# Kernel optimization log

Measured on AMD Instinct MI355X. Metric: run time of the kernel, lower is better.

The kernel has to match this reference:

```python
import jax, jax.numpy as jnp
import numpy as np

B, S, D_IN, D_OUT, H = 4, 2048, 768, 768, 12
DH = D_OUT // H


def setup_inputs() -> dict:
    key = jax.random.key(0)
    ks = jax.random.split(key, 6)
    x = jax.random.normal(ks[0], (B, S, D_IN), dtype=jnp.float32)
    # causal mask: True above the diagonal means "masked out" (filled with -inf)
    mask = jnp.triu(jnp.ones((S, S), dtype=bool), k=1)
    sc = 1.0 / np.sqrt(D_IN)
    Wq = jax.random.normal(ks[1], (D_IN, D_OUT), dtype=jnp.float32) * sc
    Wk = jax.random.normal(ks[2], (D_IN, D_OUT), dtype=jnp.float32) * sc
    Wv = jax.random.normal(ks[3], (D_IN, D_OUT), dtype=jnp.float32) * sc
    Wo = jax.random.normal(ks[4], (D_OUT, D_OUT), dtype=jnp.float32) * (1.0 / np.sqrt(D_OUT))
    bo = jnp.zeros((D_OUT,), dtype=jnp.float32)
    return {"input_tensor": x, "mask": mask, "Wq": Wq, "Wk": Wk, "Wv": Wv, "Wo": Wo, "bo": bo}


def reference(input_tensor, mask, Wq, Wk, Wv, Wo, bo):
    b, n, _ = input_tensor.shape
    # projections -> [b, h, n, dh]
    q = (input_tensor @ Wq).reshape(b, n, H, DH).transpose(0, 2, 1, 3)
    k = (input_tensor @ Wk).reshape(b, n, H, DH).transpose(0, 2, 1, 3)
    v = (input_tensor @ Wv).reshape(b, n, H, DH).transpose(0, 2, 1, 3)
    # scores [b, h, n, n]
    scores = jnp.einsum('bhqd,bhkd->bhqk', q, k)
    scores = jnp.where(mask[:n, :n], -jnp.inf, scores)
    attn = jax.nn.softmax(scores / np.sqrt(DH), axis=-1)
    ctx = jnp.einsum('bhqk,bhkd->bhqd', attn, v)
    ctx = ctx.transpose(0, 2, 1, 3).reshape(b, n, D_OUT)
    return ctx @ Wo + bo
```

## Files before the change

### kernel.cpp

```cpp
#include <hip/hip_runtime.h>
#include <hip/hip_bf16.h>
#include <math.h>

typedef __attribute__((ext_vector_type(4))) float f32x4;
typedef __attribute__((ext_vector_type(8))) short s16x8;
typedef __attribute__((ext_vector_type(8))) unsigned short u16x8;

#define B_ 4
#define S_ 2048
#define DIN 768
#define DOUT 768
#define H_ 12
#define DH_ 64
#define M_ (B_*S_)

__device__ __forceinline__ unsigned short f2bf(float f) {
  union { float f; unsigned u; } v; v.f = f;
  unsigned r = v.u + 0x7fffu + ((v.u >> 16) & 1u);
  return (unsigned short)(r >> 16);
}

#if __has_builtin(__builtin_amdgcn_exp2f)
#define EXP2(x) __builtin_amdgcn_exp2f(x)
#else
#define EXP2(x) exp2f(x)
#endif


__global__ __launch_bounds__(256) void prep(
    const float* __restrict__ X, unsigned short* __restrict__ Xb,
    const float* __restrict__ W0, const float* __restrict__ W1,
    const float* __restrict__ W2, const float* __restrict__ W3,
    unsigned short* __restrict__ Wt)
{
  __shared__ float t[32][33];
  const int bid = blockIdx.x;
  if (bid < 3072) {
    size_t i = ((size_t)bid * 256 + threadIdx.x) * 8;
    float4 a = *(const float4*)&X[i];
    float4 b = *(const float4*)&X[i + 4];
    u16x8 v;
    v[0] = f2bf(a.x); v[1] = f2bf(a.y); v[2] = f2bf(a.z); v[3] = f2bf(a.w);
    v[4] = f2bf(b.x); v[5] = f2bf(b.y); v[6] = f2bf(b.z); v[7] = f2bf(b.w);
    *(u16x8*)&Xb[i] = v;
  } else {
    const int t4 = bid - 3072;
    const int z = t4 / 576, rem = t4 - z * 576;
    const int ky = rem / 24, nx = rem - ky * 24;
    const float* W = z == 0 ? W0 : z == 1 ? W1 : z == 2 ? W2 : W3;
    unsigned short* Out = Wt + (size_t)z * DOUT * DIN;
    const int n0 = nx * 32, k0 = ky * 32;
    const int tx = threadIdx.x & 31, ty = threadIdx.x >> 5;
#pragma unroll
    for (int i = 0; i < 32; i += 8)
      t[ty + i][tx] = W[(size_t)(k0 + ty + i) * DOUT + n0 + tx];
    __syncthreads();
#pragma unroll
    for (int i = 0; i < 32; i += 8)
      Out[(size_t)(n0 + ty + i) * DIN + k0 + tx] = f2bf(t[tx][ty + i]);
  }
}


#define BKC 64
#define TILE_E (128 * BKC)

__device__ __forceinline__ void stage_tile(
    const unsigned short* __restrict__ g, int row0, int k0,
    unsigned short* lds, int tid)
{
#pragma unroll
  for (int it = 0; it < 4; ++it) {
    int s = it * 256 + tid;
    int row = s >> 3, sc = s & 7;
    int gc = sc ^ (row & 7);
    const unsigned short* gsrc = g + (size_t)(row0 + row) * 768 + k0 + gc * 8;
    unsigned short* dst = lds + (size_t)(it * 256 + (tid & ~63)) * 8;
    __builtin_amdgcn_global_load_lds(
        (const __attribute__((address_space(1))) void*)gsrc,
        (__attribute__((address_space(3))) void*)dst, 16, 0, 0);
  }
}

__device__ __forceinline__ void gemm_core(
    const unsigned short* __restrict__ A, const unsigned short* __restrict__ Bt,
    int m0, int n0, unsigned short* As, unsigned short* Bs,
    f32x4 acc[4][4], int tid)
{
  const int lane = tid & 63;
  const int col_l = lane & 15, quad = lane >> 4;
  const int w = tid >> 6;
  const int wm = (w & 1) * 64, wn = (w >> 1) * 64;

  stage_tile(A, m0, 0, As, tid);
  stage_tile(Bt, n0, 0, Bs, tid);

#pragma unroll 2
  for (int k0 = 0; k0 < 768; k0 += BKC) {
    const int cur = (k0 >> 6) & 1;
    const unsigned short* Asb = As + cur * TILE_E;
    const unsigned short* Bsb = Bs + cur * TILE_E;
    if (k0 + BKC < 768) {
      stage_tile(A, m0, k0 + BKC, As + (cur ^ 1) * TILE_E, tid);
      stage_tile(Bt, n0, k0 + BKC, Bs + (cur ^ 1) * TILE_E, tid);
      asm volatile("s_waitcnt vmcnt(8)" ::: "memory");
    } else {
      asm volatile("s_waitcnt vmcnt(0)" ::: "memory");
    }
    __builtin_amdgcn_s_barrier();

#pragma unroll
    for (int kk = 0; kk < 2; ++kk) {
      s16x8 af[4], bf[4];
#pragma unroll
      for (int t = 0; t < 4; ++t) {
        int ar = wm + t * 16 + col_l;
        af[t] = *(const s16x8*)&Asb[ar * BKC + (((kk << 2) + quad) ^ (ar & 7)) * 8];
        int br = wn + t * 16 + col_l;
        bf[t] = *(const s16x8*)&Bsb[br * BKC + (((kk << 2) + quad) ^ (br & 7)) * 8];
      }
#pragma unroll
      for (int mt = 0; mt < 4; ++mt)
#pragma unroll
        for (int nt = 0; nt < 4; ++nt)
          acc[mt][nt] = __builtin_amdgcn_mfma_f32_16x16x32_bf16(
              af[mt], bf[nt], acc[mt][nt], 0, 0, 0);
    }

    __builtin_amdgcn_s_barrier();
  }
}

__global__ __launch_bounds__(256) void proj_mfma(
    const unsigned short* __restrict__ Xb, const unsigned short* __restrict__ Wt,
    unsigned short* __restrict__ Qo, unsigned short* __restrict__ Ko,
    unsigned short* __restrict__ Vo)
{
  __shared__ unsigned short As[2 * TILE_E];
  __shared__ unsigned short Bs[2 * TILE_E];
  const int tid = threadIdx.x;

  const int orig = (blockIdx.z * 64 + blockIdx.y) * 6 + blockIdx.x;
  const int id = (orig & 7) * 144 + (orig >> 3);
  const int z = id / 384;
  const int r = id - z * 384;
  const int my = r / 6, nx = r - my * 6;
  const int m0 = my * 128, n0 = nx * 128;

  const unsigned short* Bw = Wt + (size_t)z * DOUT * DIN;
  unsigned short* Out = z == 0 ? Qo : z == 1 ? Ko : Vo;
  const float scale = z == 0 ? 0.125f * 1.44269504f : 1.0f;

  f32x4 acc[4][4] = {};
  gemm_core(Xb, Bw, m0, n0, As, Bs, acc, tid);

  const int lane = tid & 63, w = tid >> 6;
  const int col_l = lane & 15, quad = lane >> 4;
  const int wm = (w & 1) * 64, wn = (w >> 1) * 64;
  if (z == 2) {
    const int mblk = m0 + wm;
    const int b = mblk >> 11, sblk = mblk & (S_ - 1);
#pragma unroll
    for (int mt = 0; mt < 4; ++mt) {
      const int slot = (mt >> 1) * 32 + quad * 8 + (mt & 1) * 4;
#pragma unroll
      for (int nt = 0; nt < 4; ++nt) {
        int n = n0 + wn + nt * 16 + col_l;
        int h = n >> 6, d = n & 63;
        ushort4 v;
        v.x = f2bf(acc[mt][nt][0]); v.y = f2bf(acc[mt][nt][1]);
        v.z = f2bf(acc[mt][nt][2]); v.w = f2bf(acc[mt][nt][3]);
        *(ushort4*)&Out[((size_t)(b * H_ + h) * DH_ + d) * S_ + sblk + slot] = v;
      }
    }
  } else {
#pragma unroll
    for (int mt = 0; mt < 4; ++mt)
#pragma unroll
      for (int nt = 0; nt < 4; ++nt) {
        int n = n0 + wn + nt * 16 + col_l;
        int h = n >> 6, d = n & 63;
#pragma unroll
        for (int r2 = 0; r2 < 4; ++r2) {
          int m = m0 + wm + mt * 16 + quad * 4 + r2;
          int b = m >> 11, s = m & (S_ - 1);
          Out[((size_t)(b * H_ + h) * S_ + s) * DH_ + d] = f2bf(acc[mt][nt][r2] * scale);
        }
      }
  }
}

__global__ __launch_bounds__(256) void out_mfma(
    const unsigned short* __restrict__ Cb, const unsigned short* __restrict__ Wt,
    const float* __restrict__ bo, float* __restrict__ Out)
{
  __shared__ unsigned short As[2 * TILE_E];
  __shared__ unsigned short Bs[2 * TILE_E];
  const int tid = threadIdx.x;

  const int orig = blockIdx.y * 6 + blockIdx.x;
  const int id = (orig & 7) * 48 + (orig >> 3);
  const int my = id / 6, nx = id - my * 6;
  const int m0 = my * 128, n0 = nx * 128;

  f32x4 acc[4][4] = {};
  gemm_core(Cb, Wt, m0, n0, As, Bs, acc, tid);

  const int lane = tid & 63, w = tid >> 6;
  const int col_l = lane & 15, quad = lane >> 4;
  const int wm = (w & 1) * 64, wn = (w >> 1) * 64;
#pragma unroll
  for (int mt = 0; mt < 4; ++mt)
#pragma unroll
    for (int nt = 0; nt < 4; ++nt) {
      int n = n0 + wn + nt * 16 + col_l;
      float bias = bo[n];
#pragma unroll
      for (int r = 0; r < 4; ++r) {
        int m = m0 + wm + mt * 16 + quad * 4 + r;
        Out[(size_t)m * DOUT + n] = acc[mt][nt][r] + bias;
      }
    }
}


union PK { uint2 u2[2]; s16x8 v; };

#define MFMA_BF16 __builtin_amdgcn_mfma_f32_16x16x32_bf16

__device__ __forceinline__ void exppack(const f32x4 sc[4], PK& p0, PK& p1) {
#pragma unroll
  for (int nc = 0; nc < 4; ++nc) {
    float e0 = EXP2(sc[nc][0] - 17.3123405f);
    float e1 = EXP2(sc[nc][1] - 17.3123405f);
    float e2 = EXP2(sc[nc][2] - 17.3123405f);
    float e3 = EXP2(sc[nc][3] - 17.3123405f);
    union { __hip_bfloat162 v; unsigned u; } lo, hi;
    lo.v = __float22bfloat162_rn(make_float2(e0, e1));
    hi.v = __float22bfloat162_rn(make_float2(e2, e3));
    uint2 pw; pw.x = lo.u; pw.y = hi.u;
    if (nc < 2) p0.u2[nc] = pw; else p1.u2[nc - 2] = pw;
  }
}

__device__ __forceinline__ void stage_kv(
    const unsigned short* __restrict__ Kg, const unsigned short* __restrict__ Vg,
    int jn, unsigned short* KsB, unsigned short* VsB, int tid)
{
#pragma unroll
  for (int it = 0; it < 2; ++it) {
    int s = it * 256 + tid;
    int row = s >> 3;
    int gc = ((s & 7) ^ (row & 7)) * 8;
    unsigned short* dst = KsB + (size_t)(it * 256 + (tid & ~63)) * 8;
    __builtin_amdgcn_global_load_lds(
        (const __attribute__((address_space(1))) void*)(Kg + (size_t)(jn + row) * DH_ + gc),
        (__attribute__((address_space(3))) void*)dst, 16, 0, 0);
  }
#pragma unroll
  for (int it = 0; it < 2; ++it) {
    int s = it * 256 + tid;
    int row = s >> 3;
    int gc = ((s & 7) ^ (row & 7)) * 8;
    unsigned short* dst = VsB + (size_t)(it * 256 + (tid & ~63)) * 8;
    __builtin_amdgcn_global_load_lds(
        (const __attribute__((address_space(1))) void*)(Vg + (size_t)row * S_ + jn + gc),
        (__attribute__((address_space(3))) void*)dst, 16, 0, 0);
  }
}

__global__ __launch_bounds__(256, 3) void attn_mfma(
    const unsigned short* __restrict__ Q, const unsigned short* __restrict__ K,
    const unsigned short* __restrict__ Vt, unsigned short* __restrict__ CTX)
{
  __shared__ unsigned short Ks[2][64 * 64];
  __shared__ unsigned short Vs[2][64 * 64];

  const int tid = threadIdx.x;
  const int lane = tid & 63;
  const int w = tid >> 6;
  const int col_l = lane & 15;
  const int quad = lane >> 4;

  const int orig = (blockIdx.z * 12 + blockIdx.y) * 16 + blockIdx.x;
  const int id = (orig & 7) * 96 + (orig >> 3);
  const int p = id & 15;
  const int bh = id >> 4;
  const int h = bh % 12, b = bh / 12;

  const int q0A = p << 6, q0B = (31 - p) << 6;
  const int ntiles = 32 - p;
  const size_t bhs = (size_t)(b * H_ + h);
  const unsigned short* Qg = Q + bhs * S_ * DH_;
  const unsigned short* Kg = K + bhs * S_ * DH_;
  const unsigned short* Vg = Vt + bhs * DH_ * S_;

  const int qwA = q0A + (w << 4), qwB = q0B + (w << 4);
  s16x8 aqA0 = *(const s16x8*)&Qg[(size_t)(qwA + col_l) * DH_ + quad * 8];
  s16x8 aqA1 = *(const s16x8*)&Qg[(size_t)(qwA + col_l) * DH_ + 32 + quad * 8];
  s16x8 aqB0 = *(const s16x8*)&Qg[(size_t)(qwB + col_l) * DH_ + quad * 8];
  s16x8 aqB1 = *(const s16x8*)&Qg[(size_t)(qwB + col_l) * DH_ + 32 + quad * 8];

  stage_kv(Kg, Vg, 0, &Ks[0][0], &Vs[0][0], tid);

  f32x4 oA[4] = {}, oB[4] = {}, lA = {}, lB = {};
  s16x8 bones;
#pragma unroll
  for (int i = 0; i < 8; ++i) bones[i] = (short)0x3F80;

  const int qrel = (w << 4) + col_l;
  const int r7 = col_l & 7;

  for (int t = 0; t < ntiles; ++t) {
    if (t + 1 < ntiles) {
      stage_kv(Kg, Vg, (t + 1) << 6, &Ks[(t + 1) & 1][0], &Vs[(t + 1) & 1][0], tid);
      asm volatile("s_waitcnt vmcnt(4)" ::: "memory");
    } else {
      asm volatile("s_waitcnt vmcnt(0)" ::: "memory");
    }
    __builtin_amdgcn_s_barrier();

    const unsigned short* KsB = &Ks[t & 1][0];
    const unsigned short* VsB = &Vs[t & 1][0];
    const bool doA = (t <= p);

    f32x4 scA[4], scB[4];
    __builtin_amdgcn_s_setprio(1);
#pragma unroll
    for (int nc = 0; nc < 4; ++nc) {
      const int kr = nc * 16 + col_l;
      s16x8 k0 = *(const s16x8*)&KsB[kr * 64 + ((quad ^ r7) * 8)];
      s16x8 k1 = *(const s16x8*)&KsB[kr * 64 + (((quad + 4) ^ r7) * 8)];
      f32x4 a = {};
      a = MFMA_BF16(k0, aqB0, a, 0, 0, 0);
      a = MFMA_BF16(k1, aqB1, a, 0, 0, 0);
      scB[nc] = a;
      if (doA) {
        f32x4 c = {};
        c = MFMA_BF16(k0, aqA0, c, 0, 0, 0);
        c = MFMA_BF16(k1, aqA1, c, 0, 0, 0);
        scA[nc] = c;
      }
    }
    __builtin_amdgcn_s_setprio(0);
    if (t == p) {
#pragma unroll
      for (int nc = 0; nc < 4; ++nc)
#pragma unroll
        for (int r = 0; r < 4; ++r)
          if (nc * 16 + quad * 4 + r > qrel) scA[nc][r] = -INFINITY;
    }
    if (t == ntiles - 1) {
#pragma unroll
      for (int nc = 0; nc < 4; ++nc)
#pragma unroll
        for (int r = 0; r < 4; ++r)
          if (nc * 16 + quad * 4 + r > qrel) scB[nc][r] = -INFINITY;
    }

    PK pA0, pA1, pB0, pB1;
    if (doA) exppack(scA, pA0, pA1);
    exppack(scB, pB0, pB1);

    __builtin_amdgcn_s_setprio(1);
#pragma unroll
    for (int dc = 0; dc < 4; ++dc) {
      const int vr = dc * 16 + col_l;
      s16x8 b0 = *(const s16x8*)&VsB[vr * 64 + ((quad ^ r7) * 8)];
      s16x8 b1 = *(const s16x8*)&VsB[vr * 64 + (((quad + 4) ^ r7) * 8)];
      oB[dc] = MFMA_BF16(pB0.v, b0, oB[dc], 0, 0, 0);
      oB[dc] = MFMA_BF16(pB1.v, b1, oB[dc], 0, 0, 0);
      if (doA) {
        oA[dc] = MFMA_BF16(pA0.v, b0, oA[dc], 0, 0, 0);
        oA[dc] = MFMA_BF16(pA1.v, b1, oA[dc], 0, 0, 0);
      }
    }
    lB = MFMA_BF16(pB0.v, bones, lB, 0, 0, 0);
    lB = MFMA_BF16(pB1.v, bones, lB, 0, 0, 0);
    if (doA) {
      lA = MFMA_BF16(pA0.v, bones, lA, 0, 0, 0);
      lA = MFMA_BF16(pA1.v, bones, lA, 0, 0, 0);
    }
    __builtin_amdgcn_s_setprio(0);

    __builtin_amdgcn_s_barrier();
  }

  float liA[4], liB[4];
#pragma unroll
  for (int r = 0; r < 4; ++r) {
    liA[r] = 1.0f / lA[r];
    liB[r] = 1.0f / lB[r];
  }
#pragma unroll
  for (int dc = 0; dc < 4; ++dc)
#pragma unroll
    for (int r = 0; r < 4; ++r) {
      CTX[((size_t)(b * S_ + qwA + quad * 4 + r)) * DOUT + h * DH_ + dc * 16 + col_l]
          = f2bf(oA[dc][r] * liA[r]);
      CTX[((size_t)(b * S_ + qwB + quad * 4 + r)) * DOUT + h * DH_ + dc * 16 + col_l]
          = f2bf(oB[dc][r] * liB[r]);
    }
}


extern "C" void kernel_launch(void* const* d_in, const int* in_sizes, int n_in,
                              void* d_out, int out_size, void* d_ws, size_t ws_size,
                              hipStream_t stream) {
  const float* X  = (const float*)d_in[0];
  const float* Wq = (const float*)d_in[2];
  const float* Wk = (const float*)d_in[3];
  const float* Wv = (const float*)d_in[4];
  const float* Wo = (const float*)d_in[5];
  const float* bo = (const float*)d_in[6];
  float* out = (float*)d_out;

  unsigned short* Xb = (unsigned short*)d_ws;
  unsigned short* Wt = Xb + (size_t)M_ * DIN;
  unsigned short* Qb = Wt + (size_t)4 * DOUT * DIN;
  unsigned short* Kb = Qb + (size_t)M_ * DOUT;
  unsigned short* Vb = Kb + (size_t)M_ * DOUT;
  unsigned short* Cb = Vb + (size_t)M_ * DOUT;

  prep<<<dim3(3072 + 2304), 256, 0, stream>>>(X, Xb, Wq, Wk, Wv, Wo, Wt);
  proj_mfma<<<dim3(DOUT / 128, M_ / 128, 3), 256, 0, stream>>>(Xb, Wt, Qb, Kb, Vb);
  attn_mfma<<<dim3(16, H_, B_), 256, 0, stream>>>(Qb, Kb, Vb, Cb);
  out_mfma<<<dim3(DOUT / 128, M_ / 128), 256, 0, stream>>>(
      Cb, Wt + (size_t)3 * DOUT * DIN, bo, out);
}
```

Before: 196.6 us.

## Software-pipeline attention loop with triple-buffered K/V and lookahead QK+exp

Restructures the attention main loop so the QK^T scores and exponentials for tile t+1 are computed in the same iteration as the PV accumulation for tile t. K/V shared-memory staging becomes triple-buffered with a prefetch distance of two tiles, and the trailing barrier is dropped in favour of one wait+barrier per iteration. The aim is to overlap the exp/VALU work with the MFMA work and to hide global-to-LDS load latency. The cost is more LDS (three buffers instead of two) and more live registers for two sets of packed probabilities, which may reduce occupancy under the 3-blocks-per-SM launch bound. A full vmcnt(0) wait each iteration may also serialise loads.

```diff
diff --git a/kernel.cpp b/kernel.cpp
--- a/kernel.cpp
+++ b/kernel.cpp
@@ -269,12 +269,55 @@
   }
 }
 
+__device__ __forceinline__ void qk_exp(
+    const unsigned short* KsB,
+    s16x8 aqA0, s16x8 aqA1, s16x8 aqB0, s16x8 aqB1,
+    bool dA, bool maskA, bool maskB, int qrel, int col_l, int quad, int r7,
+    PK& pA0, PK& pA1, PK& pB0, PK& pB1)
+{
+  f32x4 scA[4], scB[4];
+  __builtin_amdgcn_s_setprio(1);
+#pragma unroll
+  for (int nc = 0; nc < 4; ++nc) {
+    const int kr = nc * 16 + col_l;
+    s16x8 k0 = *(const s16x8*)&KsB[kr * 64 + ((quad ^ r7) * 8)];
+    s16x8 k1 = *(const s16x8*)&KsB[kr * 64 + (((quad + 4) ^ r7) * 8)];
+    f32x4 a = {};
+    a = MFMA_BF16(k0, aqB0, a, 0, 0, 0);
+    a = MFMA_BF16(k1, aqB1, a, 0, 0, 0);
+    scB[nc] = a;
+    if (dA) {
+      f32x4 c = {};
+      c = MFMA_BF16(k0, aqA0, c, 0, 0, 0);
+      c = MFMA_BF16(k1, aqA1, c, 0, 0, 0);
+      scA[nc] = c;
+    }
+  }
+  __builtin_amdgcn_s_setprio(0);
+  if (maskA) {
+#pragma unroll
+    for (int nc = 0; nc < 4; ++nc)
+#pragma unroll
+      for (int r = 0; r < 4; ++r)
+        if (nc * 16 + quad * 4 + r > qrel) scA[nc][r] = -INFINITY;
+  }
+  if (maskB) {
+#pragma unroll
+    for (int nc = 0; nc < 4; ++nc)
+#pragma unroll
+      for (int r = 0; r < 4; ++r)
+        if (nc * 16 + quad * 4 + r > qrel) scB[nc][r] = -INFINITY;
+  }
+  if (dA) exppack(scA, pA0, pA1);
+  exppack(scB, pB0, pB1);
+}
+
 __global__ __launch_bounds__(256, 3) void attn_mfma(
     const unsigned short* __restrict__ Q, const unsigned short* __restrict__ K,
     const unsigned short* __restrict__ Vt, unsigned short* __restrict__ CTX)
 {
-  __shared__ unsigned short Ks[2][64 * 64];
-  __shared__ unsigned short Vs[2][64 * 64];
+  __shared__ unsigned short Ks[3][64 * 64];
+  __shared__ unsigned short Vs[3][64 * 64];
 
   const int tid = threadIdx.x;
   const int lane = tid & 63;
@@ -301,89 +344,66 @@
   s16x8 aqB0 = *(const s16x8*)&Qg[(size_t)(qwB + col_l) * DH_ + quad * 8];
   s16x8 aqB1 = *(const s16x8*)&Qg[(size_t)(qwB + col_l) * DH_ + 32 + quad * 8];
 
+  const int qrel = (w << 4) + col_l;
+  const int r7 = col_l & 7;
+
   stage_kv(Kg, Vg, 0, &Ks[0][0], &Vs[0][0], tid);
+  stage_kv(Kg, Vg, 64, &Ks[1][0], &Vs[1][0], tid);
+  asm volatile("s_waitcnt vmcnt(4)" ::: "memory");
+  __builtin_amdgcn_s_barrier();
+
+  PK cA0, cA1, cB0, cB1;
+  PK nA0, nA1, nB0, nB1;
+  qk_exp(&Ks[0][0], aqA0, aqA1, aqB0, aqB1,
+         true, (p == 0), (ntiles == 1),
+         qrel, col_l, quad, r7, cA0, cA1, cB0, cB1);
 
   f32x4 oA[4] = {}, oB[4] = {}, lA = {}, lB = {};
   s16x8 bones;
 #pragma unroll
   for (int i = 0; i < 8; ++i) bones[i] = (short)0x3F80;
 
-  const int qrel = (w << 4) + col_l;
-  const int r7 = col_l & 7;
+  int bc = 0, bn = 1, bs = 2;
 
   for (int t = 0; t < ntiles; ++t) {
-    if (t + 1 < ntiles) {
-      stage_kv(Kg, Vg, (t + 1) << 6, &Ks[(t + 1) & 1][0], &Vs[(t + 1) & 1][0], tid);
-      asm volatile("s_waitcnt vmcnt(4)" ::: "memory");
-    } else {
-      asm volatile("s_waitcnt vmcnt(0)" ::: "memory");
-    }
+    asm volatile("s_waitcnt vmcnt(0)" ::: "memory");
     __builtin_amdgcn_s_barrier();
 
-    const unsigned short* KsB = &Ks[t & 1][0];
-    const unsigned short* VsB = &Vs[t & 1][0];
-    const bool doA = (t <= p);
-
-    f32x4 scA[4], scB[4];
-    __builtin_amdgcn_s_setprio(1);
-#pragma unroll
-    for (int nc = 0; nc < 4; ++nc) {
-      const int kr = nc * 16 + col_l;
-      s16x8 k0 = *(const s16x8*)&KsB[kr * 64 + ((quad ^ r7) * 8)];
-      s16x8 k1 = *(const s16x8*)&KsB[kr * 64 + (((quad + 4) ^ r7) * 8)];
-      f32x4 a = {};
-      a = MFMA_BF16(k0, aqB0, a, 0, 0, 0);
-      a = MFMA_BF16(k1, aqB1, a, 0, 0, 0);
-      scB[nc] = a;
-      if (doA) {
-        f32x4 c = {};
-        c = MFMA_BF16(k0, aqA0, c, 0, 0, 0);
-        c = MFMA_BF16(k1, aqA1, c, 0, 0, 0);
-        scA[nc] = c;
-      }
-    }
-    __builtin_amdgcn_s_setprio(0);
-    if (t == p) {
-#pragma unroll
-      for (int nc = 0; nc < 4; ++nc)
-#pragma unroll
-        for (int r = 0; r < 4; ++r)
-          if (nc * 16 + quad * 4 + r > qrel) scA[nc][r] = -INFINITY;
-    }
-    if (t == ntiles - 1) {
-#pragma unroll
-      for (int nc = 0; nc < 4; ++nc)
-#pragma unroll
-        for (int r = 0; r < 4; ++r)
-          if (nc * 16 + quad * 4 + r > qrel) scB[nc][r] = -INFINITY;
-    }
-
-    PK pA0, pA1, pB0, pB1;
-    if (doA) exppack(scA, pA0, pA1);
-    exppack(scB, pB0, pB1);
-
+    if (t + 2 < ntiles)
+      stage_kv(Kg, Vg, (t + 2) << 6, &Ks[bs][0], &Vs[bs][0], tid);
+
+    const bool dA_c = (t <= p);
+
+    if (t + 1 < ntiles)
+      qk_exp(&Ks[bn][0], aqA0, aqA1, aqB0, aqB1,
+             (t + 1 <= p), (t + 1 == p),
+             (t + 1 == ntiles - 1),
+             qrel, col_l, quad, r7, nA0, nA1, nB0, nB1);
+
+    const unsigned short* VsB = &Vs[bc][0];
     __builtin_amdgcn_s_setprio(1);
 #pragma unroll
     for (int dc = 0; dc < 4; ++dc) {
       const int vr = dc * 16 + col_l;
       s16x8 b0 = *(const s16x8*)&VsB[vr * 64 + ((quad ^ r7) * 8)];
       s16x8 b1 = *(const s16x8*)&VsB[vr * 64 + (((quad + 4) ^ r7) * 8)];
-      oB[dc] = MFMA_BF16(pB0.v, b0, oB[dc], 0, 0, 0);
-      oB[dc] = MFMA_BF16(pB1.v, b1, oB[dc], 0, 0, 0);
-      if (doA) {
-        oA[dc] = MFMA_BF16(pA0.v, b0, oA[dc], 0, 0, 0);
-        oA[dc] = MFMA_BF16(pA1.v, b1, oA[dc], 0, 0, 0);
+      oB[dc] = MFMA_BF16(cB0.v, b0, oB[dc], 0, 0, 0);
+      oB[dc] = MFMA_BF16(cB1.v, b1, oB[dc], 0, 0, 0);
+      if (dA_c) {
+        oA[dc] = MFMA_BF16(cA0.v, b0, oA[dc], 0, 0, 0);
+        oA[dc] = MFMA_BF16(cA1.v, b1, oA[dc], 0, 0, 0);
       }
     }
-    lB = MFMA_BF16(pB0.v, bones, lB, 0, 0, 0);
-    lB = MFMA_BF16(pB1.v, bones, lB, 0, 0, 0);
-    if (doA) {
-      lA = MFMA_BF16(pA0.v, bones, lA, 0, 0, 0);
-      lA = MFMA_BF16(pA1.v, bones, lA, 0, 0, 0);
+    lB = MFMA_BF16(cB0.v, bones, lB, 0, 0, 0);
+    lB = MFMA_BF16(cB1.v, bones, lB, 0, 0, 0);
+    if (dA_c) {
+      lA = MFMA_BF16(cA0.v, bones, lA, 0, 0, 0);
+      lA = MFMA_BF16(cA1.v, bones, lA, 0, 0, 0);
     }
     __builtin_amdgcn_s_setprio(0);
 
-    __builtin_amdgcn_s_barrier();
+    cA0 = nA0; cA1 = nA1; cB0 = nB0; cB1 = nB1;
+    int tmp = bc; bc = bn; bn = bs; bs = tmp;
   }
 
   float liA[4], liB[4];
```

Result: no change. 199.7 us (+1.5%).

## Serialize paired query tiles into uniform 33-iteration loop instead of sharing K/V tiles

Applied to the files above, without the earlier changes.

Each block handles two causal query tiles (p and 31-p). Before, the kernel streamed 32-p K/V tiles once and computed both tiles against the shared ones. Now it runs a fixed 33 iterations: first all tiles for the B query block, then p+1 tiles again for the A query block. This gives every block an identical trip count and a single MFMA chain per iteration, which cuts divergence and register pressure. The cost is reloading p+1 K/V tiles from global memory, where before they were reused for both query tiles.

```diff
diff --git a/kernel.cpp b/kernel.cpp
--- a/kernel.cpp
+++ b/kernel.cpp
@@ -289,7 +289,8 @@
   const int h = bh % 12, b = bh / 12;
 
   const int q0A = p << 6, q0B = (31 - p) << 6;
-  const int ntiles = 32 - p;
+  const int nB = 32 - p;
+  const int NIT = 33;
   const size_t bhs = (size_t)(b * H_ + h);
   const unsigned short* Qg = Q + bhs * S_ * DH_;
   const unsigned short* Kg = K + bhs * S_ * DH_;
@@ -311,75 +312,83 @@
   const int qrel = (w << 4) + col_l;
   const int r7 = col_l & 7;
 
-  for (int t = 0; t < ntiles; ++t) {
-    if (t + 1 < ntiles) {
-      stage_kv(Kg, Vg, (t + 1) << 6, &Ks[(t + 1) & 1][0], &Vs[(t + 1) & 1][0], tid);
+  for (int i = 0; i < NIT; ++i) {
+    const int buf = i & 1;
+    if (i + 1 < NIT) {
+      const int jn_next = (i + 1 < nB ? i + 1 : i + 1 - nB) << 6;
+      stage_kv(Kg, Vg, jn_next, &Ks[buf ^ 1][0], &Vs[buf ^ 1][0], tid);
       asm volatile("s_waitcnt vmcnt(4)" ::: "memory");
     } else {
       asm volatile("s_waitcnt vmcnt(0)" ::: "memory");
     }
     __builtin_amdgcn_s_barrier();
 
-    const unsigned short* KsB = &Ks[t & 1][0];
-    const unsigned short* VsB = &Vs[t & 1][0];
-    const bool doA = (t <= p);
-
-    f32x4 scA[4], scB[4];
+    const unsigned short* KsB = &Ks[buf][0];
+    const unsigned short* VsB = &Vs[buf][0];
+    const bool isB = i < nB;
+
+    f32x4 sc[4];
     __builtin_amdgcn_s_setprio(1);
-#pragma unroll
-    for (int nc = 0; nc < 4; ++nc) {
-      const int kr = nc * 16 + col_l;
-      s16x8 k0 = *(const s16x8*)&KsB[kr * 64 + ((quad ^ r7) * 8)];
-      s16x8 k1 = *(const s16x8*)&KsB[kr * 64 + (((quad + 4) ^ r7) * 8)];
-      f32x4 a = {};
-      a = MFMA_BF16(k0, aqB0, a, 0, 0, 0);
-      a = MFMA_BF16(k1, aqB1, a, 0, 0, 0);
-      scB[nc] = a;
-      if (doA) {
-        f32x4 c = {};
-        c = MFMA_BF16(k0, aqA0, c, 0, 0, 0);
-        c = MFMA_BF16(k1, aqA1, c, 0, 0, 0);
-        scA[nc] = c;
+    if (isB) {
+#pragma unroll
+      for (int nc = 0; nc < 4; ++nc) {
+        const int kr = nc * 16 + col_l;
+        s16x8 k0 = *(const s16x8*)&KsB[kr * 64 + ((quad ^ r7) * 8)];
+        s16x8 k1 = *(const s16x8*)&KsB[kr * 64 + (((quad + 4) ^ r7) * 8)];
+        f32x4 a = {};
+        a = MFMA_BF16(k0, aqB0, a, 0, 0, 0);
+        a = MFMA_BF16(k1, aqB1, a, 0, 0, 0);
+        sc[nc] = a;
+      }
+    } else {
+#pragma unroll
+      for (int nc = 0; nc < 4; ++nc) {
+        const int kr = nc * 16 + col_l;
+        s16x8 k0 = *(const s16x8*)&KsB[kr * 64 + ((quad ^ r7) * 8)];
+        s16x8 k1 = *(const s16x8*)&KsB[kr * 64 + (((quad + 4) ^ r7) * 8)];
+        f32x4 a = {};
+        a = MFMA_BF16(k0, aqA0, a, 0, 0, 0);
+        a = MFMA_BF16(k1, aqA1, a, 0, 0, 0);
+        sc[nc] = a;
       }
     }
     __builtin_amdgcn_s_setprio(0);
-    if (t == p) {
+
+    if (i == nB - 1 || i == NIT - 1) {
 #pragma unroll
       for (int nc = 0; nc < 4; ++nc)
 #pragma unroll
         for (int r = 0; r < 4; ++r)
-          if (nc * 16 + quad * 4 + r > qrel) scA[nc][r] = -INFINITY;
-    }
-    if (t == ntiles - 1) {
-#pragma unroll
-      for (int nc = 0; nc < 4; ++nc)
-#pragma unroll
-        for (int r = 0; r < 4; ++r)
-          if (nc * 16 + quad * 4 + r > qrel) scB[nc][r] = -INFINITY;
-    }
-
-    PK pA0, pA1, pB0, pB1;
-    if (doA) exppack(scA, pA0, pA1);
-    exppack(scB, pB0, pB1);
-
-    __builtin_amdgcn_s_setprio(1);
+          if (nc * 16 + quad * 4 + r > qrel) sc[nc][r] = -INFINITY;
+    }
+
+    PK p0, p1;
+    exppack(sc, p0, p1);
+
+    s16x8 vb0[4], vb1[4];
 #pragma unroll
     for (int dc = 0; dc < 4; ++dc) {
       const int vr = dc * 16 + col_l;
-      s16x8 b0 = *(const s16x8*)&VsB[vr * 64 + ((quad ^ r7) * 8)];
-      s16x8 b1 = *(const s16x8*)&VsB[vr * 64 + (((quad + 4) ^ r7) * 8)];
-      oB[dc] = MFMA_BF16(pB0.v, b0, oB[dc], 0, 0, 0);
-      oB[dc] = MFMA_BF16(pB1.v, b1, oB[dc], 0, 0, 0);
-      if (doA) {
-        oA[dc] = MFMA_BF16(pA0.v, b0, oA[dc], 0, 0, 0);
-        oA[dc] = MFMA_BF16(pA1.v, b1, oA[dc], 0, 0, 0);
-      }
-    }
-    lB = MFMA_BF16(pB0.v, bones, lB, 0, 0, 0);
-    lB = MFMA_BF16(pB1.v, bones, lB, 0, 0, 0);
-    if (doA) {
-      lA = MFMA_BF16(pA0.v, bones, lA, 0, 0, 0);
-      lA = MFMA_BF16(pA1.v, bones, lA, 0, 0, 0);
+      vb0[dc] = *(const s16x8*)&VsB[vr * 64 + ((quad ^ r7) * 8)];
+      vb1[dc] = *(const s16x8*)&VsB[vr * 64 + (((quad + 4) ^ r7) * 8)];
+    }
+    __builtin_amdgcn_s_setprio(1);
+    if (isB) {
+#pragma unroll
+      for (int dc = 0; dc < 4; ++dc) {
+        oB[dc] = MFMA_BF16(p0.v, vb0[dc], oB[dc], 0, 0, 0);
+        oB[dc] = MFMA_BF16(p1.v, vb1[dc], oB[dc], 0, 0, 0);
+      }
+      lB = MFMA_BF16(p0.v, bones, lB, 0, 0, 0);
+      lB = MFMA_BF16(p1.v, bones, lB, 0, 0, 0);
+    } else {
+#pragma unroll
+      for (int dc = 0; dc < 4; ++dc) {
+        oA[dc] = MFMA_BF16(p0.v, vb0[dc], oA[dc], 0, 0, 0);
+        oA[dc] = MFMA_BF16(p1.v, vb1[dc], oA[dc], 0, 0, 0);
+      }
+      lA = MFMA_BF16(p0.v, bones, lA, 0, 0, 0);
+      lA = MFMA_BF16(p1.v, bones, lA, 0, 0, 0);
     }
     __builtin_amdgcn_s_setprio(0);
 
```

New measurement: 199.3 us. Within noise of the previous version (+1.3%).
